# Performance work log

Measured on AMD Instinct MI355X. Metric: run time of the kernel, lower is better.

Reference implementation:

```python
import jax, jax.numpy as jnp
import numpy as np

N, E, H, G = 50000, 500000, 64, 64


def _ln(x, g, b):
    m = jnp.mean(x, -1, keepdims=True)
    v = jnp.var(x, -1, keepdims=True)
    return (x - m) * jax.lax.rsqrt(v + 1e-5) * g + b


def _mlp_ln(x, w1, b1, w2, b2, g, be):
    # Linear -> ReLU -> (Dropout eval no-op) -> Linear -> LayerNorm
    h = jax.nn.relu(x @ w1 + b1)
    return _ln(h @ w2 + b2, g, be)


def setup_inputs() -> dict:
    key = jax.random.key(0)
    ks = jax.random.split(key, 24)
    w = lambda i, s: jax.random.normal(ks[i], s, dtype=jnp.float32) * 0.1
    z = lambda s: jnp.zeros(s, jnp.float32)
    o = lambda s: jnp.ones(s, jnp.float32)
    inp = {
        'x': jax.random.normal(ks[0], (N, 3), dtype=jnp.float32),
        'edge_index': jax.random.randint(ks[1], (2, E), 0, N),
        'edge_attr': jax.random.normal(ks[2], (E, 3), dtype=jnp.float32),
        'batch': jnp.sort(jax.random.randint(ks[3], (N,), 0, G)),
        'ne_w1': w(4, (3, H)), 'ne_b1': z((H,)), 'ne_w2': w(5, (H, H)), 'ne_b2': z((H,)), 'ne_g': o((H,)), 'ne_be': z((H,)),
        'ee_w1': w(6, (3, H)), 'ee_b1': z((H,)), 'ee_w2': w(7, (H, H)), 'ee_b2': z((H,)), 'ee_g': o((H,)), 'ee_be': z((H,)),
        'gin0_eps': z((1,)), 'gin0_w1': w(8, (H, H)), 'gin0_b1': z((H,)), 'gin0_w2': w(9, (H, H)), 'gin0_b2': z((H,)), 'gin0_g': o((H,)), 'gin0_be': z((H,)),
        'gin1_eps': z((1,)), 'gin1_w1': w(10, (H, H)), 'gin1_b1': z((H,)), 'gin1_w2': w(11, (H, H)), 'gin1_b2': z((H,)), 'gin1_g': o((H,)), 'gin1_be': z((H,)),
        'gp_w': w(12, (H, H)), 'gp_b': z((H,)), 'gp_g': o((H,)), 'gp_be': z((H,)),
        'ep_w1': w(13, (4 * H, 2 * H)), 'ep_b1': z((2 * H,)),
        'ep_w2': w(14, (2 * H, H)), 'ep_b2': z((H,)),
        'ep_w3': w(15, (H, 1)), 'ep_b3': z((1,)),
    }
    return inp


def reference(x, edge_index, edge_attr, batch,
              ne_w1, ne_b1, ne_w2, ne_b2, ne_g, ne_be,
              ee_w1, ee_b1, ee_w2, ee_b2, ee_g, ee_be,
              gin0_eps, gin0_w1, gin0_b1, gin0_w2, gin0_b2, gin0_g, gin0_be,
              gin1_eps, gin1_w1, gin1_b1, gin1_w2, gin1_b2, gin1_g, gin1_be,
              gp_w, gp_b, gp_g, gp_be,
              ep_w1, ep_b1, ep_w2, ep_b2, ep_w3, ep_b3):
    src, dst = edge_index[0], edge_index[1]
    # encoders
    h = _mlp_ln(x, ne_w1, ne_b1, ne_w2, ne_b2, ne_g, ne_be)            # [N, H]
    ef = _mlp_ln(edge_attr, ee_w1, ee_b1, ee_w2, ee_b2, ee_g, ee_be)   # [E, H]
    # GINEConv layer 0: mlp((1+eps)*x + scatter_add(relu(x_src + e)))
    msg = jax.nn.relu(h[src] + ef)
    aggr = jnp.zeros_like(h).at[dst].add(msg)
    h = _mlp_ln((1.0 + gin0_eps) * h + aggr, gin0_w1, gin0_b1, gin0_w2, gin0_b2, gin0_g, gin0_be)
    h = jax.nn.relu(h)  # inter-layer activation (dropout eval no-op)
    # GINEConv layer 1
    msg = jax.nn.relu(h[src] + ef)
    aggr = jnp.zeros_like(h).at[dst].add(msg)
    h = _mlp_ln((1.0 + gin1_eps) * h + aggr, gin1_w1, gin1_b1, gin1_w2, gin1_b2, gin1_g, gin1_be)
    # global mean pool over graphs
    seg = jax.ops.segment_sum(h, batch, num_segments=G)                            # [G, H]
    cnt = jax.ops.segment_sum(jnp.ones((h.shape[0], 1), h.dtype), batch, num_segments=G)
    gp = seg / jnp.maximum(cnt, 1.0)
    gf = _ln(jax.nn.relu(gp @ gp_w + gp_b), gp_g, gp_be)                           # [G, H]
    # edge predictor on [src | dst | global | edge] = [E, 4H]
    c = jnp.concatenate([h[src], h[dst], gf[batch[src]], ef], axis=-1)
    t = jnp.tanh(c @ ep_w1 + ep_b1)
    t = jnp.tanh(t @ ep_w2 + ep_b2)
    return jax.nn.sigmoid(t @ ep_w3 + ep_b3)  # [E, 1]
```

## Files before the change

kernel.cpp:

```cpp
#include <hip/hip_runtime.h>
#include <hip/hip_bf16.h>

typedef unsigned int uint;
typedef unsigned short ushort;
typedef __attribute__((ext_vector_type(8))) short short8;
typedef __attribute__((ext_vector_type(4))) float floatx4;

__device__ __forceinline__ float bf2f(ushort u) { return __uint_as_float(((uint)u) << 16); }
__device__ __forceinline__ ushort f2bf(float f) {
  uint u = __float_as_uint(f);
  u += 0x7fffu + ((u >> 16) & 1u);
  return (ushort)(u >> 16);
}
__device__ __forceinline__ uint pk2(float a, float b) {
  return (uint)f2bf(a) | ((uint)f2bf(b) << 16);
}
__device__ __forceinline__ float ldf(const void* p, long i, int m) {
  if (m) return bf2f(((const ushort*)p)[i]);
  return ((const float*)p)[i];
}
__device__ __forceinline__ int get_md(const uint* mdp) {
  return (mdp[0] == 0x3F800000u) ? 0 : 1;
}
__device__ __forceinline__ float fast_rcp(float x) { return __builtin_amdgcn_rcpf(x); }
__device__ __forceinline__ float tanh_fast(float x) {
  float e = __builtin_amdgcn_exp2f(2.8853900818f * x);
  return fmaf(-2.f, fast_rcp(1.f + e), 1.f);
}
__device__ __forceinline__ float sigmoid_fast(float x) {
  float e = __builtin_amdgcn_exp2f(-1.4426950409f * x);
  return fast_rcp(1.f + e);
}

__global__ __launch_bounds__(256) void k_enc_mfma(
    const void* __restrict__ in, int R,
    const void* __restrict__ w1, const void* __restrict__ b1,
    const ushort* __restrict__ w2sw_, const void* __restrict__ b2,
    const void* __restrict__ gam, const void* __restrict__ bet,
    ushort* __restrict__ outp, const uint* __restrict__ mdp)
{
  __shared__ float xs[64*3];
  __shared__ float w1s[192], b1s[64], b2s[64], gs[64], bs2[64];
  __shared__ __align__(16) ushort T_s[64 * 72];
  int md = get_md(mdp);
  int tid = threadIdx.x;
  long e0 = (long)blockIdx.x * 64;
  if (tid < 192) {
    w1s[tid] = ldf(w1, tid, md);
    int row = tid / 3, cc = tid - row*3;
    long e = e0 + row;
    xs[tid] = (e < R) ? ldf(in, e*3 + cc, md) : 0.f;
  }
  if (tid < 64) { b1s[tid] = ldf(b1, tid, md); b2s[tid] = ldf(b2, tid, md);
                  gs[tid] = ldf(gam, tid, md); bs2[tid] = ldf(bet, tid, md); }
  __syncthreads();
  int lane = tid & 63, wv = tid >> 6;
  int quad = lane >> 4, mm = lane & 15;
  float x0 = xs[(wv*16 + mm)*3 + 0];
  float x1 = xs[(wv*16 + mm)*3 + 1];
  float x2 = xs[(wv*16 + mm)*3 + 2];
  short8 af[2];
#pragma unroll
  for (int s = 0; s < 2; ++s) {
#pragma unroll
    for (int j = 0; j < 8; ++j) {
      int f = s*32 + quad*8 + j;
      float hv = fmaxf(b1s[f] + x0*w1s[f] + x1*w1s[64+f] + x2*w1s[128+f], 0.f);
      af[s][j] = (short)f2bf(hv);
    }
  }
  floatx4 acc[4] = {};
  const short8* Bp = (const short8*)w2sw_;
#pragma unroll
  for (int s = 0; s < 2; ++s) {
#pragma unroll
    for (int t = 0; t < 4; ++t) {
      short8 b = Bp[(s*4 + t)*64 + lane];
      acc[t] = __builtin_amdgcn_mfma_f32_16x16x32_bf16(af[s], b, acc[t], 0, 0, 0);
    }
  }
  float vv[4][4];
#pragma unroll
  for (int t = 0; t < 4; ++t) {
    float bb = b2s[mm + 16*t];
#pragma unroll
    for (int r = 0; r < 4; ++r) vv[t][r] = acc[t][r] + bb;
  }
  float mr[4], vr[4];
#pragma unroll
  for (int r = 0; r < 4; ++r) {
    float s = vv[0][r] + vv[1][r] + vv[2][r] + vv[3][r];
#pragma unroll
    for (int off = 1; off < 16; off <<= 1) s += __shfl_xor(s, off);
    mr[r] = s * 0.015625f;
    float q = 0.f;
#pragma unroll
    for (int t = 0; t < 4; ++t) { float d = vv[t][r] - mr[r]; q = fmaf(d, d, q); }
#pragma unroll
    for (int off = 1; off < 16; off <<= 1) q += __shfl_xor(q, off);
    vr[r] = rsqrtf(q * 0.015625f + 1e-5f);
  }
#pragma unroll
  for (int t = 0; t < 4; ++t) {
    int col = mm + 16*t;
    float g = gs[col], be = bs2[col];
#pragma unroll
    for (int r = 0; r < 4; ++r)
      T_s[(wv*16 + quad*4 + r)*72 + col] = f2bf((vv[t][r] - mr[r]) * vr[r] * g + be);
  }
  __syncthreads();
#pragma unroll
  for (int i = 0; i < 2; ++i) {
    int gi = tid + 256*i;
    int row = gi >> 3, c = gi & 7;
    long e = e0 + row;
    if (e < R)
      ((uint4*)(outp + e*64))[c] = *(const uint4*)&T_s[row*72 + c*8];
  }
}

__global__ __launch_bounds__(256) void k_deg(
    const int* __restrict__ ei, int* __restrict__ deg, int E_)
{
  int e = blockIdx.x * 256 + threadIdx.x;
  if (e < E_) atomicAdd(&deg[ei[E_ + e]], 1);
}

__global__ __launch_bounds__(256) void k_scan1(
    const int* __restrict__ deg, int* __restrict__ rs, int* __restrict__ bsum, int Nn)
{
  __shared__ int ls[256];
  int tid = threadIdx.x;
  int i = blockIdx.x * 256 + tid;
  int v = (i < Nn) ? deg[i] : 0;
  ls[tid] = v;
  __syncthreads();
  for (int off = 1; off < 256; off <<= 1) {
    int t = (tid >= off) ? ls[tid - off] : 0;
    __syncthreads();
    ls[tid] += t;
    __syncthreads();
  }
  if (i < Nn) rs[i] = ls[tid] - v;
  if (tid == 255) bsum[blockIdx.x] = ls[255];
}

__global__ __launch_bounds__(256) void k_scan2(
    int* __restrict__ bsum, int nb, int* __restrict__ rs, int Nn)
{
  __shared__ int ls[256];
  int tid = threadIdx.x;
  int chunk = (nb + 255) / 256;
  int c0 = tid * chunk, c1 = min(c0 + chunk, nb);
  int sum = 0;
  for (int i = c0; i < c1; ++i) sum += bsum[i];
  ls[tid] = sum;
  __syncthreads();
  for (int off = 1; off < 256; off <<= 1) {
    int t = (tid >= off) ? ls[tid - off] : 0;
    __syncthreads();
    ls[tid] += t;
    __syncthreads();
  }
  int run = ls[tid] - sum;
  for (int i = c0; i < c1; ++i) { int d = bsum[i]; bsum[i] = run; run += d; }
  if (tid == 255) rs[Nn] = ls[255];
}

__global__ __launch_bounds__(256) void k_scan3(
    int* __restrict__ rs, int* __restrict__ cur,
    const int* __restrict__ bsum, int Nn)
{
  int i = blockIdx.x * 256 + threadIdx.x;
  if (i < Nn) {
    int v = rs[i] + bsum[blockIdx.x];
    rs[i] = v;
    cur[i] = v;
  }
}

__global__ __launch_bounds__(256) void k_fill(
    const int* __restrict__ ei, int* __restrict__ cur, int* __restrict__ eidx, int E_)
{
  int e = blockIdx.x * 256 + threadIdx.x;
  if (e < E_) {
    int d = ei[E_ + e];
    int p = atomicAdd(&cur[d], 1);
    eidx[p] = e;
  }
}

__global__ __launch_bounds__(256) void k_aggr(
    const ushort* __restrict__ hbu, const ushort* __restrict__ efu,
    const int* __restrict__ ei, const int* __restrict__ rs,
    const int* __restrict__ eidx, float* __restrict__ aggr, int Nn, int E_)
{
  int gw = (blockIdx.x * 256 + threadIdx.x) >> 6;
  int j = threadIdx.x & 63;
  if (gw >= Nn) return;
  int s0 = rs[gw], s1 = rs[gw + 1];
  float acc = 0.f;
  int idx = s0;
  for (; idx + 2 <= s1; idx += 2) {
    int e1 = eidx[idx], e2 = eidx[idx + 1];
    int sA = ei[e1], sB = ei[e2];
    float hA = bf2f(hbu[(long)sA*64 + j]);
    float fA = bf2f(efu[(long)e1*64 + j]);
    float hB = bf2f(hbu[(long)sB*64 + j]);
    float fB = bf2f(efu[(long)e2*64 + j]);
    acc += fmaxf(hA + fA, 0.f) + fmaxf(hB + fB, 0.f);
  }
  if (idx < s1) {
    int e1 = eidx[idx];
    int sA = ei[e1];
    acc += fmaxf(bf2f(hbu[(long)sA*64 + j]) + bf2f(efu[(long)e1*64 + j]), 0.f);
  }
  aggr[(long)gw*64 + j] = acc;
}

__global__ __launch_bounds__(256) void k_gine_mfma(
    const ushort* __restrict__ hbin, const float* __restrict__ aggr, int Nn,
    const void* __restrict__ epsp,
    const ushort* __restrict__ w1sw_, const void* __restrict__ b1,
    const ushort* __restrict__ w2sw_, const void* __restrict__ b2,
    const void* __restrict__ gam, const void* __restrict__ bet,
    ushort* __restrict__ hbout, int post_relu, const uint* __restrict__ mdp)
{
  __shared__ __align__(16) ushort Ws1[4096], Ws2[4096];
  __shared__ __align__(16) ushort T_s[64 * 72];
  __shared__ float b1s[64], b2s[64], gs[64], bs2[64];
  int md = get_md(mdp);
  int tid = threadIdx.x;
  {
    const uint4* p1 = (const uint4*)w1sw_;
    const uint4* p2 = (const uint4*)w2sw_;
    ((uint4*)Ws1)[tid] = p1[tid];
    ((uint4*)Ws1)[tid + 256] = p1[tid + 256];
    ((uint4*)Ws2)[tid] = p2[tid];
    ((uint4*)Ws2)[tid + 256] = p2[tid + 256];
  }
  if (tid < 64) { b1s[tid] = ldf(b1, tid, md); b2s[tid] = ldf(b2, tid, md);
                  gs[tid] = ldf(gam, tid, md); bs2[tid] = ldf(bet, tid, md); }
  float ope = 1.f + ldf(epsp, 0, md);
  int lane = tid & 63, wv = tid >> 6;
  int quad = lane >> 4, mm = lane & 15;
  long node = (long)blockIdx.x * 64 + wv*16 + mm;
  long nc = (node < Nn) ? node : (long)(Nn - 1);
  const ushort* hrow = hbin + nc*64;
  const float*  arow = aggr + nc*64;
  short8 af[2];
#pragma unroll
  for (int s = 0; s < 2; ++s) {
    int c = s*4 + quad;
    short8 hv = *(const short8*)(hrow + c*8);
    float4 a0 = *(const float4*)(arow + c*8);
    float4 a1 = *(const float4*)(arow + c*8 + 4);
    float uu[8];
    uu[0] = fmaf(bf2f((ushort)hv[0]), ope, a0.x);
    uu[1] = fmaf(bf2f((ushort)hv[1]), ope, a0.y);
    uu[2] = fmaf(bf2f((ushort)hv[2]), ope, a0.z);
    uu[3] = fmaf(bf2f((ushort)hv[3]), ope, a0.w);
    uu[4] = fmaf(bf2f((ushort)hv[4]), ope, a1.x);
    uu[5] = fmaf(bf2f((ushort)hv[5]), ope, a1.y);
    uu[6] = fmaf(bf2f((ushort)hv[6]), ope, a1.z);
    uu[7] = fmaf(bf2f((ushort)hv[7]), ope, a1.w);
#pragma unroll
    for (int j = 0; j < 8; ++j) af[s][j] = (short)f2bf(uu[j]);
  }
  __syncthreads();
  floatx4 acc[4] = {};
#pragma unroll
  for (int s = 0; s < 2; ++s) {
#pragma unroll
    for (int t = 0; t < 4; ++t) {
      short8 b = *(const short8*)&Ws1[((s*4 + t)*64 + lane)*8];
      acc[t] = __builtin_amdgcn_mfma_f32_16x16x32_bf16(af[s], b, acc[t], 0, 0, 0);
    }
  }
#pragma unroll
  for (int t = 0; t < 4; ++t) {
    int col = mm + 16*t;
    float bb = b1s[col];
#pragma unroll
    for (int r = 0; r < 4; ++r)
      T_s[(wv*16 + quad*4 + r)*72 + col] = f2bf(fmaxf(acc[t][r] + bb, 0.f));
  }
  __syncthreads();
  short8 af2[2];
#pragma unroll
  for (int s = 0; s < 2; ++s)
    af2[s] = *(const short8*)&T_s[(wv*16 + mm)*72 + s*32 + quad*8];
  floatx4 acc2[4] = {};
#pragma unroll
  for (int s = 0; s < 2; ++s) {
#pragma unroll
    for (int t = 0; t < 4; ++t) {
      short8 b = *(const short8*)&Ws2[((s*4 + t)*64 + lane)*8];
      acc2[t] = __builtin_amdgcn_mfma_f32_16x16x32_bf16(af2[s], b, acc2[t], 0, 0, 0);
    }
  }
  float vv[4][4];
#pragma unroll
  for (int t = 0; t < 4; ++t) {
    float bb = b2s[mm + 16*t];
#pragma unroll
    for (int r = 0; r < 4; ++r) vv[t][r] = acc2[t][r] + bb;
  }
  float mr[4], vr[4];
#pragma unroll
  for (int r = 0; r < 4; ++r) {
    float s = vv[0][r] + vv[1][r] + vv[2][r] + vv[3][r];
#pragma unroll
    for (int off = 1; off < 16; off <<= 1) s += __shfl_xor(s, off);
    mr[r] = s * 0.015625f;
    float q = 0.f;
#pragma unroll
    for (int t = 0; t < 4; ++t) { float d = vv[t][r] - mr[r]; q = fmaf(d, d, q); }
#pragma unroll
    for (int off = 1; off < 16; off <<= 1) q += __shfl_xor(q, off);
    vr[r] = rsqrtf(q * 0.015625f + 1e-5f);
  }
  __syncthreads();
#pragma unroll
  for (int t = 0; t < 4; ++t) {
    int col = mm + 16*t;
    float g = gs[col], be = bs2[col];
#pragma unroll
    for (int r = 0; r < 4; ++r) {
      float o = (vv[t][r] - mr[r]) * vr[r] * g + be;
      if (post_relu) o = fmaxf(o, 0.f);
      T_s[(wv*16 + quad*4 + r)*72 + col] = f2bf(o);
    }
  }
  __syncthreads();
#pragma unroll
  for (int i = 0; i < 2; ++i) {
    int gi = tid + 256*i;
    int row = gi >> 3, c = gi & 7;
    long n2 = (long)blockIdx.x * 64 + row;
    if (n2 < Nn)
      ((uint4*)(hbout + n2*64))[c] = *(const uint4*)&T_s[row*72 + c*8];
  }
}

__global__ __launch_bounds__(256) void k_pool_f(
    const ushort* __restrict__ hbu, const int* __restrict__ batch,
    float* __restrict__ gsum, float* __restrict__ gcnt, int Nn)
{
  int gw = (blockIdx.x * 256 + threadIdx.x) >> 6;
  int j = threadIdx.x & 63;
  long r0 = (long)gw * 64;
  if (r0 >= Nn) return;
  long rend = min(r0 + 64, (long)Nn);
  float acc = 0.f; int cur = batch[r0]; int run = 0;
  for (long r = r0; r < rend; ++r) {
    int g = batch[r];
    if (g != cur) {
      atomicAdd(&gsum[cur*64 + j], acc);
      if (j == 0) atomicAdd(&gcnt[cur], (float)run);
      acc = 0.f; run = 0; cur = g;
    }
    acc += bf2f(hbu[r*64 + j]);
    run++;
  }
  atomicAdd(&gsum[cur*64 + j], acc);
  if (j == 0) atomicAdd(&gcnt[cur], (float)run);
}

__global__ __launch_bounds__(64) void k_pool_fin_f(
    const float* __restrict__ gsum, const float* __restrict__ gcnt,
    const void* __restrict__ gpw, const void* __restrict__ gpb,
    const void* __restrict__ gpg, const void* __restrict__ gpbe,
    ushort* __restrict__ gfb, const uint* __restrict__ mdp)
{
  __shared__ float wgs[4096];
  __shared__ float us[64];
  int md = get_md(mdp);
  int j = threadIdx.x;
  int g = blockIdx.x;
  for (int i = j; i < 4096; i += 64) wgs[i] = ldf(gpw, i, md);
  float ic = 1.f / fmaxf(gcnt[g], 1.f);
  us[j] = gsum[g*64 + j] * ic;
  __syncthreads();
  float t = ldf(gpb, j, md);
#pragma unroll
  for (int k = 0; k < 64; ++k) t = fmaf(us[k], wgs[k*64 + j], t);
  t = fmaxf(t, 0.f);
  float m = t;
#pragma unroll
  for (int off = 1; off < 64; off <<= 1) m += __shfl_xor(m, off);
  m *= 0.015625f;
  float d = t - m;
  float v = d * d;
#pragma unroll
  for (int off = 1; off < 64; off <<= 1) v += __shfl_xor(v, off);
  float rs = rsqrtf(v * 0.015625f + 1e-5f);
  gfb[g*64 + j] = f2bf(d * rs * ldf(gpg, j, md) + ldf(gpbe, j, md));
}

__global__ __launch_bounds__(256) void k_swz(
    const void* __restrict__ w1, const void* __restrict__ w2,
    const void* __restrict__ w2e, const void* __restrict__ w2n,
    const void* __restrict__ gw10, const void* __restrict__ gw20,
    const void* __restrict__ gw11, const void* __restrict__ gw21,
    ushort* __restrict__ w1sw, ushort* __restrict__ w2sw,
    ushort* __restrict__ ew2sw, ushort* __restrict__ nw2sw,
    ushort* __restrict__ g0w1sw, ushort* __restrict__ g0w2sw,
    ushort* __restrict__ g1w1sw, ushort* __restrict__ g1w2sw,
    const uint* __restrict__ mdp)
{
  int md = get_md(mdp);
  int i = blockIdx.x * 256 + threadIdx.x;
  if (i < 32768) {
    int q = i & 7, lane = (i >> 3) & 63, tt = (i >> 9) & 7, s = i >> 12;
    int k = s*32 + (lane >> 4)*8 + q, n = (lane & 15) + 16*tt;
    w1sw[i] = f2bf(ldf(w1, k*128 + n, md));
  }
  if (i < 8192) {
    int q = i & 7, lane = (i >> 3) & 63, tt = (i >> 9) & 3, s = i >> 11;
    int k = s*32 + (lane >> 4)*8 + q, n = (lane & 15) + 16*tt;
    int src = k*64 + n;
    w2sw[i]   = f2bf(ldf(w2,   src, md));
    ew2sw[i]  = f2bf(ldf(w2e,  src, md));
    nw2sw[i]  = f2bf(ldf(w2n,  src, md));
    g0w1sw[i] = f2bf(ldf(gw10, src, md));
    g0w2sw[i] = f2bf(ldf(gw20, src, md));
    g1w1sw[i] = f2bf(ldf(gw11, src, md));
    g1w2sw[i] = f2bf(ldf(gw21, src, md));
  }
}

__global__ __launch_bounds__(256) void k_pred_mfma(
    const ushort* __restrict__ hb, const ushort* __restrict__ efu,
    const ushort* __restrict__ gfb, const int* __restrict__ ei,
    const int* __restrict__ batch,
    const ushort* __restrict__ w1sw, const ushort* __restrict__ w2sw,
    const void* __restrict__ pb1, const void* __restrict__ pb2,
    const void* __restrict__ pw3, const void* __restrict__ pb3,
    void* __restrict__ out, int E_, const uint* __restrict__ mdp)
{
  __shared__ __align__(16) ushort Ws[8192];
  __shared__ __align__(16) ushort T_s[64 * 136];
  __shared__ float b1s[128], b2s[64], w3s[64];
  int md = get_md(mdp);
  int tid = threadIdx.x;
  if (tid < 128) b1s[tid] = ldf(pb1, tid, md);
  if (tid < 64) { b2s[tid] = ldf(pb2, tid, md); w3s[tid] = ldf(pw3, tid, md); }
  long e0 = (long)blockIdx.x * 64;
  int lane = tid & 63, wv = tid >> 6;
  int quad = lane >> 4, mm = lane & 15;
  long e = e0 + wv*16 + mm;
  if (e >= E_) e = E_ - 1;
  int si = ei[e];
  int di = ei[E_ + e];
  int gi = batch[si];
  const short8* hsrc = (const short8*)(hb  + (long)si*64);
  const short8* hdst = (const short8*)(hb  + (long)di*64);
  const short8* gsrc = (const short8*)(gfb + (long)gi*64);
  const short8* esrc = (const short8*)(efu + e*64);
  short8 af[8];
  af[0] = hsrc[quad]; af[1] = hsrc[4 + quad];
  af[2] = hdst[quad]; af[3] = hdst[4 + quad];
  af[4] = gsrc[quad]; af[5] = gsrc[4 + quad];
  af[6] = esrc[quad]; af[7] = esrc[4 + quad];
  floatx4 acc[8] = {};
  for (int q = 0; q < 4; ++q) {
    __syncthreads();
    const uint4* wp = (const uint4*)(w1sw + q*8192);
#pragma unroll
    for (int i = 0; i < 4; ++i)
      ((uint4*)Ws)[tid + 256*i] = wp[tid + 256*i];
    __syncthreads();
#pragma unroll
    for (int s4 = 0; s4 < 2; ++s4) {
      short8 a = af[q*2 + s4];
#pragma unroll
      for (int t = 0; t < 8; ++t) {
        short8 b = *(const short8*)&Ws[((s4*8 + t)*64 + lane)*8];
        acc[t] = __builtin_amdgcn_mfma_f32_16x16x32_bf16(a, b, acc[t], 0, 0, 0);
      }
    }
  }
#pragma unroll
  for (int t = 0; t < 8; ++t) {
    float bb = b1s[mm + 16*t];
#pragma unroll
    for (int r = 0; r < 4; ++r)
      T_s[(16*wv + quad*4 + r)*136 + mm + 16*t] = f2bf(tanh_fast(acc[t][r] + bb));
  }
  __syncthreads();
  {
    const uint4* wp2 = (const uint4*)w2sw;
#pragma unroll
    for (int i = 0; i < 4; ++i)
      ((uint4*)Ws)[tid + 256*i] = wp2[tid + 256*i];
  }
  __syncthreads();
  floatx4 acc2[4] = {};
#pragma unroll
  for (int s2 = 0; s2 < 4; ++s2) {
    short8 a = *(const short8*)&T_s[(16*wv + mm)*136 + s2*32 + quad*8];
#pragma unroll
    for (int t = 0; t < 4; ++t) {
      short8 b = *(const short8*)&Ws[((s2*4 + t)*64 + lane)*8];
      acc2[t] = __builtin_amdgcn_mfma_f32_16x16x32_bf16(a, b, acc2[t], 0, 0, 0);
    }
  }
  float p0 = 0.f, p1 = 0.f, p2 = 0.f, p3 = 0.f;
#pragma unroll
  for (int t = 0; t < 4; ++t) {
    int col = mm + 16*t;
    float bb = b2s[col], w3v = w3s[col];
    p0 = fmaf(tanh_fast(acc2[t][0] + bb), w3v, p0);
    p1 = fmaf(tanh_fast(acc2[t][1] + bb), w3v, p1);
    p2 = fmaf(tanh_fast(acc2[t][2] + bb), w3v, p2);
    p3 = fmaf(tanh_fast(acc2[t][3] + bb), w3v, p3);
  }
#pragma unroll
  for (int off = 1; off < 16; off <<= 1) {
    p0 += __shfl_xor(p0, off);
    p1 += __shfl_xor(p1, off);
    p2 += __shfl_xor(p2, off);
    p3 += __shfl_xor(p3, off);
  }
  if (mm == 0) {
    float b3 = ldf(pb3, 0, md);
    long eb = e0 + 16*wv + quad*4;
    float ps[4] = {p0, p1, p2, p3};
#pragma unroll
    for (int r = 0; r < 4; ++r) {
      if (eb + r < E_) {
        float sg = sigmoid_fast(ps[r] + b3);
        if (md) ((ushort*)out)[eb + r] = f2bf(sg);
        else    ((float*)out)[eb + r]  = sg;
      }
    }
  }
}

extern "C" void kernel_launch(void* const* d_in, const int* in_sizes, int n_in,
                              void* d_out, int out_size, void* d_ws, size_t ws_size,
                              hipStream_t stream)
{
  const void* x     = d_in[0];
  const int*  ei    = (const int*)d_in[1];
  const void* eattr = d_in[2];
  const int*  batch = (const int*)d_in[3];
  const void* ne_w1 = d_in[4];  const void* ne_b1 = d_in[5];
  const void* ne_w2 = d_in[6];  const void* ne_b2 = d_in[7];
  const void* ne_g  = d_in[8];  const void* ne_be = d_in[9];
  const void* ee_w1 = d_in[10]; const void* ee_b1 = d_in[11];
  const void* ee_w2 = d_in[12]; const void* ee_b2 = d_in[13];
  const void* ee_g  = d_in[14]; const void* ee_be = d_in[15];
  const void* g0_ep = d_in[16];
  const void* g0_w1 = d_in[17]; const void* g0_b1 = d_in[18];
  const void* g0_w2 = d_in[19]; const void* g0_b2 = d_in[20];
  const void* g0_g  = d_in[21]; const void* g0_be = d_in[22];
  const void* g1_ep = d_in[23];
  const void* g1_w1 = d_in[24]; const void* g1_b1 = d_in[25];
  const void* g1_w2 = d_in[26]; const void* g1_b2 = d_in[27];
  const void* g1_g  = d_in[28]; const void* g1_be = d_in[29];
  const void* gp_w  = d_in[30]; const void* gp_b  = d_in[31];
  const void* gp_g  = d_in[32]; const void* gp_be = d_in[33];
  const void* ep_w1 = d_in[34]; const void* ep_b1 = d_in[35];
  const void* ep_w2 = d_in[36]; const void* ep_b2 = d_in[37];
  const void* ep_w3 = d_in[38]; const void* ep_b3 = d_in[39];

  int N = in_sizes[3];
  int E = in_sizes[1] / 2;
  const uint* mdp = (const uint*)ne_g;

  char* ws = (char*)d_ws;
  size_t off = 0;
  auto alloc = [&](size_t bytes) { char* p = ws + off; off += (bytes + 255) & ~(size_t)255; return p; };
  ushort* hb     = (ushort*)alloc((size_t)N * 64 * 2);
  ushort* efu    = (ushort*)alloc((size_t)E * 64 * 2);
  float*  aggr   = (float*) alloc((size_t)N * 64 * 4);
  float*  gsum   = (float*) alloc(64 * 64 * 4);
  float*  gcnt   = (float*) alloc(64 * 4);
  ushort* gfb    = (ushort*)alloc(64 * 64 * 2);
  ushort* w1sw   = (ushort*)alloc(32768 * 2);
  ushort* w2sw   = (ushort*)alloc(8192 * 2);
  ushort* ew2sw  = (ushort*)alloc(8192 * 2);
  ushort* nw2sw  = (ushort*)alloc(8192 * 2);
  ushort* g0w1sw = (ushort*)alloc(8192 * 2);
  ushort* g0w2sw = (ushort*)alloc(8192 * 2);
  ushort* g1w1sw = (ushort*)alloc(8192 * 2);
  ushort* g1w2sw = (ushort*)alloc(8192 * 2);
  int*    deg    = (int*)   alloc((size_t)N * 4);
  int*    rs     = (int*)   alloc((size_t)(N + 1) * 4);
  int*    cur    = (int*)   alloc((size_t)N * 4);
  int*    eidx   = (int*)   alloc((size_t)E * 4);
  int*    bsum   = (int*)   alloc((size_t)((N + 255) / 256) * 4);
  (void)ws_size; (void)n_in; (void)out_size;

  int gN = (N + 255) / 256;
  int gE = (E + 255) / 256;
  int gE64 = (E + 63) / 64;
  int gN64 = (N + 63) / 64;
  int gAggr = (int)(((long)N * 64 + 255) / 256);
  int gPool = ((N + 63) / 64 + 3) / 4;

  hipMemsetAsync(deg, 0, (size_t)N * 4, stream);
  hipMemsetAsync(gsum, 0, 64 * 64 * 4 + 256, stream);

  k_swz<<<128, 256, 0, stream>>>(ep_w1, ep_w2, ee_w2, ne_w2, g0_w1, g0_w2, g1_w1, g1_w2,
                                 w1sw, w2sw, ew2sw, nw2sw,
                                 g0w1sw, g0w2sw, g1w1sw, g1w2sw, mdp);
  k_deg<<<gE, 256, 0, stream>>>(ei, deg, E);
  k_scan1<<<gN, 256, 0, stream>>>(deg, rs, bsum, N);
  k_scan2<<<1, 256, 0, stream>>>(bsum, gN, rs, N);
  k_scan3<<<gN, 256, 0, stream>>>(rs, cur, bsum, N);
  k_fill<<<gE, 256, 0, stream>>>(ei, cur, eidx, E);
  k_enc_mfma<<<gN64, 256, 0, stream>>>(x, N, ne_w1, ne_b1, nw2sw, ne_b2, ne_g, ne_be, hb, mdp);
  k_enc_mfma<<<gE64, 256, 0, stream>>>(eattr, E, ee_w1, ee_b1, ew2sw, ee_b2, ee_g, ee_be, efu, mdp);
  k_aggr<<<gAggr, 256, 0, stream>>>(hb, efu, ei, rs, eidx, aggr, N, E);
  k_gine_mfma<<<gN64, 256, 0, stream>>>(hb, aggr, N, g0_ep, g0w1sw, g0_b1, g0w2sw, g0_b2,
                                        g0_g, g0_be, hb, 1, mdp);
  k_aggr<<<gAggr, 256, 0, stream>>>(hb, efu, ei, rs, eidx, aggr, N, E);
  k_gine_mfma<<<gN64, 256, 0, stream>>>(hb, aggr, N, g1_ep, g1w1sw, g1_b1, g1w2sw, g1_b2,
                                        g1_g, g1_be, hb, 0, mdp);
  k_pool_f<<<gPool, 256, 0, stream>>>(hb, batch, gsum, gcnt, N);
  k_pool_fin_f<<<64, 64, 0, stream>>>(gsum, gcnt, gp_w, gp_b, gp_g, gp_be, gfb, mdp);
  k_pred_mfma<<<gE64, 256, 0, stream>>>(hb, efu, gfb, ei, batch, w1sw, w2sw,
                                        ep_b1, ep_b2, ep_w3, ep_b3, d_out, E, mdp);
}
```

Measured before the change: 475.6 us.

## Store edge features in dst-sorted order and pack edge/src pairs for aggregation

```diff
diff --git a/kernel.cpp b/kernel.cpp
--- a/kernel.cpp
+++ b/kernel.cpp
@@ -37,7 +37,8 @@
     const void* __restrict__ w1, const void* __restrict__ b1,
     const ushort* __restrict__ w2sw_, const void* __restrict__ b2,
     const void* __restrict__ gam, const void* __restrict__ bet,
-    ushort* __restrict__ outp, const uint* __restrict__ mdp)
+    ushort* __restrict__ outp, ushort* __restrict__ outp2,
+    const int* __restrict__ epos, const uint* __restrict__ mdp)
 {
   __shared__ float xs[64*3];
   __shared__ float w1s[192], b1s[64], b2s[64], gs[64], bs2[64];
@@ -114,8 +115,48 @@
     int gi = tid + 256*i;
     int row = gi >> 3, c = gi & 7;
     long e = e0 + row;
-    if (e < R)
-      ((uint4*)(outp + e*64))[c] = *(const uint4*)&T_s[row*72 + c*8];
+    if (e < R) {
+      uint4 v = *(const uint4*)&T_s[row*72 + c*8];
+      ((uint4*)(outp + e*64))[c] = v;
+      if (outp2)
+        ((uint4*)(outp2 + (long)epos[e]*64))[c] = v;
+    }
+  }
+}
+
+__global__ __launch_bounds__(256) void k_swz(
+    const void* __restrict__ w1, const void* __restrict__ w2,
+    const void* __restrict__ w2e, const void* __restrict__ w2n,
+    const void* __restrict__ gw10, const void* __restrict__ gw20,
+    const void* __restrict__ gw11, const void* __restrict__ gw21,
+    ushort* __restrict__ w1sw, ushort* __restrict__ w2sw,
+    ushort* __restrict__ ew2sw, ushort* __restrict__ nw2sw,
+    ushort* __restrict__ g0w1sw, ushort* __restrict__ g0w2sw,
+    ushort* __restrict__ g1w1sw, ushort* __restrict__ g1w2sw,
+    int* __restrict__ deg, float* __restrict__ gsum, int Nn,
+    const uint* __restrict__ mdp)
+{
+  int md = get_md(mdp);
+  int i = blockIdx.x * 256 + threadIdx.x;
+  int nthr = gridDim.x * 256;
+  for (int k = i; k < Nn; k += nthr) deg[k] = 0;
+  for (int k = i; k < 64*64 + 64; k += nthr) gsum[k] = 0.f;
+  if (i < 32768) {
+    int q = i & 7, lane = (i >> 3) & 63, tt = (i >> 9) & 7, s = i >> 12;
+    int k = s*32 + (lane >> 4)*8 + q, n = (lane & 15) + 16*tt;
+    w1sw[i] = f2bf(ldf(w1, k*128 + n, md));
+  }
+  if (i < 8192) {
+    int q = i & 7, lane = (i >> 3) & 63, tt = (i >> 9) & 3, s = i >> 11;
+    int k = s*32 + (lane >> 4)*8 + q, n = (lane & 15) + 16*tt;
+    int src = k*64 + n;
+    w2sw[i]   = f2bf(ldf(w2,   src, md));
+    ew2sw[i]  = f2bf(ldf(w2e,  src, md));
+    nw2sw[i]  = f2bf(ldf(w2n,  src, md));
+    g0w1sw[i] = f2bf(ldf(gw10, src, md));
+    g0w2sw[i] = f2bf(ldf(gw20, src, md));
+    g1w1sw[i] = f2bf(ldf(gw11, src, md));
+    g1w2sw[i] = f2bf(ldf(gw21, src, md));
   }
 }
 
@@ -180,20 +221,23 @@
 }
 
 __global__ __launch_bounds__(256) void k_fill(
-    const int* __restrict__ ei, int* __restrict__ cur, int* __restrict__ eidx, int E_)
+    const int* __restrict__ ei, int* __restrict__ cur,
+    int2* __restrict__ ep, int* __restrict__ epos, int E_)
 {
   int e = blockIdx.x * 256 + threadIdx.x;
   if (e < E_) {
+    int s = ei[e];
     int d = ei[E_ + e];
     int p = atomicAdd(&cur[d], 1);
-    eidx[p] = e;
+    ep[p] = make_int2(e, s);
+    epos[e] = p;
   }
 }
 
 __global__ __launch_bounds__(256) void k_aggr(
-    const ushort* __restrict__ hbu, const ushort* __restrict__ efu,
-    const int* __restrict__ ei, const int* __restrict__ rs,
-    const int* __restrict__ eidx, float* __restrict__ aggr, int Nn, int E_)
+    const ushort* __restrict__ hbu, const ushort* __restrict__ efp,
+    const int2* __restrict__ ep, const int* __restrict__ rs,
+    float* __restrict__ aggr, int Nn)
 {
   int gw = (blockIdx.x * 256 + threadIdx.x) >> 6;
   int j = threadIdx.x & 63;
@@ -202,18 +246,17 @@
   float acc = 0.f;
   int idx = s0;
   for (; idx + 2 <= s1; idx += 2) {
-    int e1 = eidx[idx], e2 = eidx[idx + 1];
-    int sA = ei[e1], sB = ei[e2];
-    float hA = bf2f(hbu[(long)sA*64 + j]);
-    float fA = bf2f(efu[(long)e1*64 + j]);
-    float hB = bf2f(hbu[(long)sB*64 + j]);
-    float fB = bf2f(efu[(long)e2*64 + j]);
+    int2 a = ep[idx];
+    int2 b = ep[idx + 1];
+    float fA = bf2f(efp[(long)idx*64 + j]);
+    float fB = bf2f(efp[(long)(idx+1)*64 + j]);
+    float hA = bf2f(hbu[(long)a.y*64 + j]);
+    float hB = bf2f(hbu[(long)b.y*64 + j]);
     acc += fmaxf(hA + fA, 0.f) + fmaxf(hB + fB, 0.f);
   }
   if (idx < s1) {
-    int e1 = eidx[idx];
-    int sA = ei[e1];
-    acc += fmaxf(bf2f(hbu[(long)sA*64 + j]) + bf2f(efu[(long)e1*64 + j]), 0.f);
+    int2 a = ep[idx];
+    acc += fmaxf(bf2f(hbu[(long)a.y*64 + j]) + bf2f(efp[(long)idx*64 + j]), 0.f);
   }
   aggr[(long)gw*64 + j] = acc;
 }
@@ -396,38 +439,6 @@
   for (int off = 1; off < 64; off <<= 1) v += __shfl_xor(v, off);
   float rs = rsqrtf(v * 0.015625f + 1e-5f);
   gfb[g*64 + j] = f2bf(d * rs * ldf(gpg, j, md) + ldf(gpbe, j, md));
-}
-
-__global__ __launch_bounds__(256) void k_swz(
-    const void* __restrict__ w1, const void* __restrict__ w2,
-    const void* __restrict__ w2e, const void* __restrict__ w2n,
-    const void* __restrict__ gw10, const void* __restrict__ gw20,
-    const void* __restrict__ gw11, const void* __restrict__ gw21,
-    ushort* __restrict__ w1sw, ushort* __restrict__ w2sw,
-    ushort* __restrict__ ew2sw, ushort* __restrict__ nw2sw,
-    ushort* __restrict__ g0w1sw, ushort* __restrict__ g0w2sw,
-    ushort* __restrict__ g1w1sw, ushort* __restrict__ g1w2sw,
-    const uint* __restrict__ mdp)
-{
-  int md = get_md(mdp);
-  int i = blockIdx.x * 256 + threadIdx.x;
-  if (i < 32768) {
-    int q = i & 7, lane = (i >> 3) & 63, tt = (i >> 9) & 7, s = i >> 12;
-    int k = s*32 + (lane >> 4)*8 + q, n = (lane & 15) + 16*tt;
-    w1sw[i] = f2bf(ldf(w1, k*128 + n, md));
-  }
-  if (i < 8192) {
-    int q = i & 7, lane = (i >> 3) & 63, tt = (i >> 9) & 3, s = i >> 11;
-    int k = s*32 + (lane >> 4)*8 + q, n = (lane & 15) + 16*tt;
-    int src = k*64 + n;
-    w2sw[i]   = f2bf(ldf(w2,   src, md));
-    ew2sw[i]  = f2bf(ldf(w2e,  src, md));
-    nw2sw[i]  = f2bf(ldf(w2n,  src, md));
-    g0w1sw[i] = f2bf(ldf(gw10, src, md));
-    g0w2sw[i] = f2bf(ldf(gw20, src, md));
-    g1w1sw[i] = f2bf(ldf(gw11, src, md));
-    g1w2sw[i] = f2bf(ldf(gw21, src, md));
-  }
 }
 
 __global__ __launch_bounds__(256) void k_pred_mfma(
@@ -575,9 +586,10 @@
   auto alloc = [&](size_t bytes) { char* p = ws + off; off += (bytes + 255) & ~(size_t)255; return p; };
   ushort* hb     = (ushort*)alloc((size_t)N * 64 * 2);
   ushort* efu    = (ushort*)alloc((size_t)E * 64 * 2);
+  ushort* efp    = (ushort*)alloc((size_t)E * 64 * 2);
   float*  aggr   = (float*) alloc((size_t)N * 64 * 4);
-  float*  gsum   = (float*) alloc(64 * 64 * 4);
-  float*  gcnt   = (float*) alloc(64 * 4);
+  float*  gsum   = (float*) alloc((64 * 64 + 64) * 4);
+  float*  gcnt   = gsum + 64 * 64;
   ushort* gfb    = (ushort*)alloc(64 * 64 * 2);
   ushort* w1sw   = (ushort*)alloc(32768 * 2);
   ushort* w2sw   = (ushort*)alloc(8192 * 2);
@@ -590,7 +602,8 @@
   int*    deg    = (int*)   alloc((size_t)N * 4);
   int*    rs     = (int*)   alloc((size_t)(N + 1) * 4);
   int*    cur    = (int*)   alloc((size_t)N * 4);
-  int*    eidx   = (int*)   alloc((size_t)E * 4);
+  int2*   ep     = (int2*)  alloc((size_t)E * 8);
+  int*    epos   = (int*)   alloc((size_t)E * 4);
   int*    bsum   = (int*)   alloc((size_t)((N + 255) / 256) * 4);
   (void)ws_size; (void)n_in; (void)out_size;
 
@@ -601,23 +614,23 @@
   int gAggr = (int)(((long)N * 64 + 255) / 256);
   int gPool = ((N + 63) / 64 + 3) / 4;
 
-  hipMemsetAsync(deg, 0, (size_t)N * 4, stream);
-  hipMemsetAsync(gsum, 0, 64 * 64 * 4 + 256, stream);
-
   k_swz<<<128, 256, 0, stream>>>(ep_w1, ep_w2, ee_w2, ne_w2, g0_w1, g0_w2, g1_w1, g1_w2,
                                  w1sw, w2sw, ew2sw, nw2sw,
-                                 g0w1sw, g0w2sw, g1w1sw, g1w2sw, mdp);
+                                 g0w1sw, g0w2sw, g1w1sw, g1w2sw,
+                                 deg, gsum, N, mdp);
   k_deg<<<gE, 256, 0, stream>>>(ei, deg, E);
   k_scan1<<<gN, 256, 0, stream>>>(deg, rs, bsum, N);
   k_scan2<<<1, 256, 0, stream>>>(bsum, gN, rs, N);
   k_scan3<<<gN, 256, 0, stream>>>(rs, cur, bsum, N);
-  k_fill<<<gE, 256, 0, stream>>>(ei, cur, eidx, E);
-  k_enc_mfma<<<gN64, 256, 0, stream>>>(x, N, ne_w1, ne_b1, nw2sw, ne_b2, ne_g, ne_be, hb, mdp);
-  k_enc_mfma<<<gE64, 256, 0, stream>>>(eattr, E, ee_w1, ee_b1, ew2sw, ee_b2, ee_g, ee_be, efu, mdp);
-  k_aggr<<<gAggr, 256, 0, stream>>>(hb, efu, ei, rs, eidx, aggr, N, E);
+  k_fill<<<gE, 256, 0, stream>>>(ei, cur, ep, epos, E);
+  k_enc_mfma<<<gN64, 256, 0, stream>>>(x, N, ne_w1, ne_b1, nw2sw, ne_b2, ne_g, ne_be,
+                                       hb, (ushort*)nullptr, (const int*)nullptr, mdp);
+  k_enc_mfma<<<gE64, 256, 0, stream>>>(eattr, E, ee_w1, ee_b1, ew2sw, ee_b2, ee_g, ee_be,
+                                       efu, efp, epos, mdp);
+  k_aggr<<<gAggr, 256, 0, stream>>>(hb, efp, ep, rs, aggr, N);
   k_gine_mfma<<<gN64, 256, 0, stream>>>(hb, aggr, N, g0_ep, g0w1sw, g0_b1, g0w2sw, g0_b2,
                                         g0_g, g0_be, hb, 1, mdp);
-  k_aggr<<<gAggr, 256, 0, stream>>>(hb, efu, ei, rs, eidx, aggr, N, E);
+  k_aggr<<<gAggr, 256, 0, stream>>>(hb, efp, ep, rs, aggr, N);
   k_gine_mfma<<<gN64, 256, 0, stream>>>(hb, aggr, N, g1_ep, g1w1sw, g1_b1, g1w2sw, g1_b2,
                                         g1_g, g1_be, hb, 0, mdp);
   k_pool_f<<<gPool, 256, 0, stream>>>(hb, batch, gsum, gcnt, N);
```

After: 456.9 us. 3.9% less time.
